# Optimization experiments

Hardware: AMD Instinct MI355X
Metric: run time of the kernel (lower is better)

The kernel has to match this reference:

```python
import jax, jax.numpy as jnp
import numpy as np

N_HEADS, N_LEVELS, N_POINTS, D_MODEL = 8, 4, 4, 256
HEAD_DIM = D_MODEL // N_HEADS
SHAPES = [(96, 96), (48, 48), (24, 24), (12, 12)]


def setup_inputs() -> dict:
    key = jax.random.key(0)
    ks = jax.random.split(key, 9)
    shapes_np = np.asarray(SHAPES, dtype=np.int32)
    lengths = shapes_np[:, 0] * shapes_np[:, 1]
    Len = int(lengths.sum())  # 12240
    B = 1
    level_start = np.concatenate([[0], np.cumsum(lengths)[:-1]]).astype(np.int32)
    return {
        "query": jax.random.normal(ks[0], (B, Len, D_MODEL), jnp.float32),
        "reference_points": jax.random.uniform(ks[1], (B, Len, 2), jnp.float32),
        "input_flatten": jax.random.normal(ks[2], (B, Len, D_MODEL), jnp.float32),
        "spatial_shapes": jnp.asarray(shapes_np),
        "level_start_index": jnp.asarray(level_start),
        "W_off": jax.random.normal(ks[3], (D_MODEL, N_HEADS * N_LEVELS * N_POINTS * 2), jnp.float32) * 0.01,
        "b_off": jax.random.normal(ks[4], (N_HEADS * N_LEVELS * N_POINTS * 2,), jnp.float32) * 0.01,
        "W_attn": jax.random.normal(ks[5], (D_MODEL, N_HEADS * N_LEVELS * N_POINTS), jnp.float32) * 0.02,
        "b_attn": jnp.zeros((N_HEADS * N_LEVELS * N_POINTS,), jnp.float32),
        "W_out": jax.random.normal(ks[6], (D_MODEL, D_MODEL), jnp.float32) * 0.02,
        "b_out": jnp.zeros((D_MODEL,), jnp.float32),
    }


def _bilinear_gather(feat, x, y, H, W):
    """feat: [B,nH,H*W,D]; x,y: [B,nH,S] pixel coords. Zero padding, align_corners=False."""
    x0 = jnp.floor(x)
    y0 = jnp.floor(y)
    wx1 = x - x0
    wy1 = y - y0
    wx0 = 1.0 - wx1
    wy0 = 1.0 - wy1
    x0i = x0.astype(jnp.int32)
    y0i = y0.astype(jnp.int32)

    def corner(ix, iy):
        valid = (ix >= 0) & (ix < W) & (iy >= 0) & (iy < H)
        idx = jnp.clip(iy, 0, H - 1) * W + jnp.clip(ix, 0, W - 1)
        g = jnp.take_along_axis(feat, idx[..., None], axis=2)  # [B,nH,S,D]
        return g * valid[..., None].astype(feat.dtype)

    return (corner(x0i, y0i) * (wx0 * wy0)[..., None]
            + corner(x0i + 1, y0i) * (wx1 * wy0)[..., None]
            + corner(x0i, y0i + 1) * (wx0 * wy1)[..., None]
            + corner(x0i + 1, y0i + 1) * (wx1 * wy1)[..., None])


def _ms_deform_core(value, shapes_np, loc, attn):
    """value: [B,Len_in,nH,D]; loc: [B,LQ,nH,nL,nP,2]; attn: [B,LQ,nH,nL,nP]."""
    B, LQ = loc.shape[0], loc.shape[1]
    lengths = [int(h) * int(w) for h, w in shapes_np]
    starts = np.concatenate([[0], np.cumsum(lengths)])
    out = jnp.zeros((B, N_HEADS, LQ, HEAD_DIM), value.dtype)
    for lvl, (H, W) in enumerate(shapes_np):
        H, W = int(H), int(W)
        feat = value[:, starts[lvl]:starts[lvl + 1]].transpose(0, 2, 1, 3)  # [B,nH,HW,D]
        l = loc[:, :, :, lvl]  # [B,LQ,nH,nP,2]
        x = (l[..., 0] * W - 0.5).transpose(0, 2, 1, 3).reshape(B, N_HEADS, LQ * N_POINTS)
        y = (l[..., 1] * H - 0.5).transpose(0, 2, 1, 3).reshape(B, N_HEADS, LQ * N_POINTS)
        samp = _bilinear_gather(feat, x, y, H, W).reshape(B, N_HEADS, LQ, N_POINTS, HEAD_DIM)
        w = attn[:, :, :, lvl].transpose(0, 2, 1, 3)  # [B,nH,LQ,nP]
        out = out + (samp * w[..., None]).sum(axis=3)
    return out.transpose(0, 2, 1, 3).reshape(B, LQ, N_HEADS * HEAD_DIM)


def reference(query, reference_points, input_flatten, spatial_shapes, level_start_index,
              W_off, b_off, W_attn, b_attn, W_out, b_out):
    B, LQ, C = query.shape
    shapes_np = np.asarray(spatial_shapes)  # static per-level (H,W)
    off = (query @ W_off + b_off).reshape(B, LQ, N_HEADS, N_LEVELS, N_POINTS, 2)
    attn = jax.nn.softmax((query @ W_attn + b_attn).reshape(B, LQ, N_HEADS, N_LEVELS * N_POINTS), axis=-1)
    attn = attn.reshape(B, LQ, N_HEADS, N_LEVELS, N_POINTS)
    # offset_normalizer = (W, H) per level
    norm = jnp.asarray(np.stack([shapes_np[:, 1], shapes_np[:, 0]], -1), dtype=query.dtype)
    loc = reference_points[:, :, None, None, None, :] + off / norm[None, None, None, :, None, :]
    value = input_flatten.reshape(B, -1, N_HEADS, HEAD_DIM)
    out = _ms_deform_core(value, shapes_np, loc, attn)
    return out @ W_out + b_out
```

## Files before the change

kernel.cpp:

```cpp
#include <hip/hip_runtime.h>
#include <hip/hip_bf16.h>
#include <math.h>

constexpr int D_MODEL  = 256;
constexpr int N_HEADS  = 8;

typedef __attribute__((ext_vector_type(8))) short bf16x8;
typedef __attribute__((ext_vector_type(4))) float f32x4;

__device__ __forceinline__ void gld_lds16(const void* gsrc, void* ldst) {
    __builtin_amdgcn_global_load_lds(
        (const __attribute__((address_space(1))) unsigned int*)gsrc,
        (__attribute__((address_space(3))) unsigned int*)ldst, 16, 0, 0);
}

__global__ __launch_bounds__(256) void convert_kernel(
    const float* __restrict__ q,
    const float* __restrict__ Woff,
    const float* __restrict__ Wattn,
    const float* __restrict__ Wout,
    __hip_bfloat16* __restrict__ qbf,
    __hip_bfloat16* __restrict__ wt,
    int M)
{
    int t = blockIdx.x * 256 + threadIdx.x;
    int nq4 = M * 64;
    if (t < nq4) {
        float4 v = reinterpret_cast<const float4*>(q)[t];
        union { __hip_bfloat16 h[4]; ushort4 u; } cv;
        cv.h[0] = __float2bfloat16(v.x);
        cv.h[1] = __float2bfloat16(v.y);
        cv.h[2] = __float2bfloat16(v.z);
        cv.h[3] = __float2bfloat16(v.w);
        reinterpret_cast<ushort4*>(qbf)[t] = cv.u;
    } else {
        int t2 = t - nq4;
        if (t2 < 640 * 256) {
            int c = t2 >> 8, k = t2 & 255;
            float val = (c < 256) ? Woff[k * 256 + c]
                      : (c < 384) ? Wattn[k * 128 + (c - 256)]
                                  : Wout[k * 256 + (c - 384)];
            wt[c * 256 + k] = __float2bfloat16(val);
        }
    }
}

template <int EPI>
__global__ __launch_bounds__(256) void gemm_mfma(
    const __hip_bfloat16* __restrict__ Abf,
    const __hip_bfloat16* __restrict__ Wt,
    int wrow0,
    const float* __restrict__ ba,
    const float* __restrict__ bb,
    const float* __restrict__ refpts,
    float* __restrict__ out0,
    float* __restrict__ out1,
    int M)
{
    __shared__ __align__(16) char smem[128 * 68 * 4];
    char*  A_lds = smem;
    char*  B_lds = smem + 16384;
    float* C_lds = (float*)smem;

    const int tid = threadIdx.x;
    const int w = tid >> 6, l = tid & 63;
    const int m0 = blockIdx.y * 128;
    const int n0 = blockIdx.x * 64;

    const char* Asrc = (const char*)Abf;
    const char* Wsrc = (const char*)(Wt + (size_t)(wrow0 + n0) * 256);

    f32x4 acc[2][4] = {};

    const int lr8 = l >> 3, l7 = l & 7;

    for (int k0 = 0; k0 < 512; k0 += 128) {
#pragma unroll
        for (int i = 0; i < 4; ++i) {
            int chunk = (w << 2) + i;
            int row = (chunk << 3) + lr8;
            int m = m0 + row; m = m < M ? m : (M - 1);
            gld_lds16(Asrc + (size_t)m * 512 + k0 + ((l7 ^ (row & 7)) << 4),
                      A_lds + (chunk << 10));
        }
#pragma unroll
        for (int i = 0; i < 2; ++i) {
            int chunk = (w << 1) + i;
            int row = (chunk << 3) + lr8;
            gld_lds16(Wsrc + (size_t)row * 512 + k0 + ((l7 ^ (row & 7)) << 4),
                      B_lds + (chunk << 10));
        }
        __syncthreads();

#pragma unroll
        for (int kk = 0; kk < 2; ++kk) {
            bf16x8 av[2], bv[4];
#pragma unroll
            for (int mf = 0; mf < 2; ++mf) {
                int arow = (w << 5) + (mf << 4) + (l & 15);
                int acb = ((kk << 6) + ((l >> 4) << 4)) ^ ((arow & 7) << 4);
                av[mf] = *(const bf16x8*)(A_lds + arow * 128 + acb);
            }
#pragma unroll
            for (int nf = 0; nf < 4; ++nf) {
                int brow = (nf << 4) + (l & 15);
                int bcb = ((kk << 6) + ((l >> 4) << 4)) ^ ((brow & 7) << 4);
                bv[nf] = *(const bf16x8*)(B_lds + brow * 128 + bcb);
            }
#pragma unroll
            for (int mf = 0; mf < 2; ++mf)
#pragma unroll
                for (int nf = 0; nf < 4; ++nf)
                    acc[mf][nf] = __builtin_amdgcn_mfma_f32_16x16x32_bf16(
                        av[mf], bv[nf], acc[mf][nf], 0, 0, 0);
        }
        __syncthreads();
    }

#pragma unroll
    for (int mf = 0; mf < 2; ++mf)
#pragma unroll
        for (int nf = 0; nf < 4; ++nf) {
            int col = (nf << 4) + (l & 15);
            int rbase = (w << 5) + (mf << 4) + ((l >> 4) << 2);
#pragma unroll
            for (int j = 0; j < 4; ++j)
                C_lds[(rbase + j) * 68 + col] = acc[mf][nf][j];
        }
    __syncthreads();

    if (EPI == 0 || n0 < 256) {
#pragma unroll
        for (int r2 = 0; r2 < 2; ++r2) {
            int row = (r2 << 6) + (tid >> 2);
            int q = m0 + row;
            if (q >= M) continue;
            float rx = 0.f, ry = 0.f;
            if (EPI == 1) { rx = refpts[q * 2]; ry = refpts[q * 2 + 1]; }
#pragma unroll
            for (int g = 0; g < 4; ++g) {
                int col = ((tid & 3) << 4) + (g << 2);
                float4 v  = *(float4*)&C_lds[row * 68 + col];
                float4 b4 = *(const float4*)&ba[n0 + col];
                if (EPI == 0) {
                    v.x += b4.x; v.y += b4.y; v.z += b4.z; v.w += b4.w;
                } else {
                    int c = n0 + col;
                    float rn = 1.0f / (float)(96 >> ((c >> 3) & 3));
                    v.x = rx + (v.x + b4.x) * rn;
                    v.y = ry + (v.y + b4.y) * rn;
                    v.z = rx + (v.z + b4.z) * rn;
                    v.w = ry + (v.w + b4.w) * rn;
                }
                *(float4*)&out0[(size_t)q * 256 + n0 + col] = v;
            }
        }
    } else {
        for (int u = tid; u < 512; u += 256) {
            int row = u >> 2, hh = u & 3;
            int q = m0 + row;
            if (q >= M) continue;
            int cg = (n0 - 256) + (hh << 4);
            float s[16];
            float mx = -1e30f;
#pragma unroll
            for (int i = 0; i < 16; ++i) {
                s[i] = C_lds[row * 68 + (hh << 4) + i] + bb[cg + i];
                mx = fmaxf(mx, s[i]);
            }
            float sum = 0.f;
#pragma unroll
            for (int i = 0; i < 16; ++i) { s[i] = __expf(s[i] - mx); sum += s[i]; }
            float inv = 1.0f / sum;
#pragma unroll
            for (int g = 0; g < 4; ++g) {
                float4 v = make_float4(s[g*4]*inv, s[g*4+1]*inv, s[g*4+2]*inv, s[g*4+3]*inv);
                *(float4*)&out1[(size_t)q * 128 + cg + (g << 2)] = v;
            }
        }
    }
}

__global__ __launch_bounds__(256, 4) void sample_kernel(
    const float* __restrict__ loc,
    const float* __restrict__ attn,
    const float* __restrict__ value,
    __hip_bfloat16* __restrict__ core,
    int M)
{
    const int unit = blockIdx.x * 32 + (threadIdx.x >> 3);
    const int d4   = threadIdx.x & 7;
    const int q    = unit >> 3;
    const int h    = unit & 7;
    if (q >= M) return;

    const float4* locq4 = reinterpret_cast<const float4*>(loc  + (size_t)q * 256 + h * 32);
    const float4* attq4 = reinterpret_cast<const float4*>(attn + (size_t)q * 128 + h * 16);
    const float*  vbase = value + h * 32 + d4 * 4;

    float4 acc = make_float4(0.f, 0.f, 0.f, 0.f);

#pragma unroll 1
    for (int lvl = 0; lvl < 4; ++lvl) {
        const int Wl = 96 >> lvl;
        const int start = 12288 - (12288 >> (2 * lvl));
        const float fW = (float)Wl;
        const int rowstride = Wl * 256;
        const float* feat = vbase + (size_t)start * 256;

        float4 lp0 = locq4[lvl * 2 + 0];
        float4 lp1 = locq4[lvl * 2 + 1];
        float4 aw  = attq4[lvl];

        const float lxs[4] = {lp0.x, lp0.z, lp1.x, lp1.z};
        const float lys[4] = {lp0.y, lp0.w, lp1.y, lp1.w};
        const float aws[4] = {aw.x, aw.y, aw.z, aw.w};

#pragma unroll
        for (int p = 0; p < 4; ++p) {
            float x = lxs[p] * fW - 0.5f;
            float y = lys[p] * fW - 0.5f;
            float wgt = aws[p];

            float x0f = floorf(x);
            float y0f = floorf(y);
            float wx1 = x - x0f, wy1 = y - y0f;
            float wx0 = 1.f - wx1, wy0 = 1.f - wy1;
            int ix = (int)x0f;
            int iy = (int)y0f;

            float wxv0 = ((unsigned)ix       < (unsigned)Wl) ? wx0 : 0.f;
            float wxv1 = ((unsigned)(ix + 1) < (unsigned)Wl) ? wx1 : 0.f;
            float wyv0 = (((unsigned)iy       < (unsigned)Wl) ? wy0 : 0.f) * wgt;
            float wyv1 = (((unsigned)(iy + 1) < (unsigned)Wl) ? wy1 : 0.f) * wgt;

            int ix0 = min(max(ix,     0), Wl - 1);
            int ix1 = min(max(ix + 1, 0), Wl - 1);
            int iy0 = min(max(iy,     0), Wl - 1);
            int iy1 = min(max(iy + 1, 0), Wl - 1);

            const float* row0 = feat + (size_t)iy0 * rowstride;
            const float* row1 = feat + (size_t)iy1 * rowstride;
            float4 v00 = *reinterpret_cast<const float4*>(&row0[(size_t)ix0 * 256]);
            float4 v10 = *reinterpret_cast<const float4*>(&row0[(size_t)ix1 * 256]);
            float4 v01 = *reinterpret_cast<const float4*>(&row1[(size_t)ix0 * 256]);
            float4 v11 = *reinterpret_cast<const float4*>(&row1[(size_t)ix1 * 256]);

            float w00 = wxv0 * wyv0, w10 = wxv1 * wyv0;
            float w01 = wxv0 * wyv1, w11 = wxv1 * wyv1;

            acc.x = fmaf(v00.x, w00, acc.x); acc.x = fmaf(v10.x, w10, acc.x);
            acc.x = fmaf(v01.x, w01, acc.x); acc.x = fmaf(v11.x, w11, acc.x);
            acc.y = fmaf(v00.y, w00, acc.y); acc.y = fmaf(v10.y, w10, acc.y);
            acc.y = fmaf(v01.y, w01, acc.y); acc.y = fmaf(v11.y, w11, acc.y);
            acc.z = fmaf(v00.z, w00, acc.z); acc.z = fmaf(v10.z, w10, acc.z);
            acc.z = fmaf(v01.z, w01, acc.z); acc.z = fmaf(v11.z, w11, acc.z);
            acc.w = fmaf(v00.w, w00, acc.w); acc.w = fmaf(v10.w, w10, acc.w);
            acc.w = fmaf(v01.w, w01, acc.w); acc.w = fmaf(v11.w, w11, acc.w);
        }
    }

    union { __hip_bfloat16 h4[4]; ushort4 u4; } st;
    st.h4[0] = __float2bfloat16(acc.x);
    st.h4[1] = __float2bfloat16(acc.y);
    st.h4[2] = __float2bfloat16(acc.z);
    st.h4[3] = __float2bfloat16(acc.w);
    *reinterpret_cast<ushort4*>(core + ((size_t)q * 256 + h * 32 + d4 * 4)) = st.u4;
}

extern "C" void kernel_launch(void* const* d_in, const int* in_sizes, int n_in,
                              void* d_out, int out_size, void* d_ws, size_t ws_size,
                              hipStream_t stream)
{
    const float* query  = (const float*)d_in[0];
    const float* refp   = (const float*)d_in[1];
    const float* value  = (const float*)d_in[2];
    const float* W_off  = (const float*)d_in[5];
    const float* b_off  = (const float*)d_in[6];
    const float* W_attn = (const float*)d_in[7];
    const float* b_attn = (const float*)d_in[8];
    const float* W_out  = (const float*)d_in[9];
    const float* b_out  = (const float*)d_in[10];
    float* out = (float*)d_out;

    const int M = in_sizes[0] / D_MODEL;

    float* loc  = (float*)d_ws;
    float* attn = loc + (size_t)M * 256;
    __hip_bfloat16* qbf = (__hip_bfloat16*)(attn + (size_t)M * 128);
    __hip_bfloat16* wt  = qbf + (size_t)M * 256;
    __hip_bfloat16* core = qbf;

    dim3 blk(256);
    const int mblocks = (M + 127) / 128;

    int convthreads = M * 64 + 640 * 256;
    hipLaunchKernelGGL(convert_kernel, dim3((convthreads + 255) / 256), blk, 0, stream,
                       query, W_off, W_attn, W_out, qbf, wt, M);

    hipLaunchKernelGGL((gemm_mfma<1>), dim3(6, mblocks), blk, 0, stream,
                       qbf, wt, 0, b_off, b_attn, refp, loc, attn, M);

    const int units = M * N_HEADS;
    hipLaunchKernelGGL(sample_kernel, dim3((units + 31) / 32), blk, 0, stream,
                       loc, attn, value, core, M);

    hipLaunchKernelGGL((gemm_mfma<0>), dim3(4, mblocks), blk, 0, stream,
                       core, wt, 384, b_out, nullptr, nullptr, out, nullptr, M);
}
```

Before: 73.57 us.

## Transpose value into per-head planes and schedule sampling blocks by head

The convert kernel now also copies the value tensor into a head-major layout, [head][pixel][32], so each head's features are contiguous. The sampling kernel reads from these planes and each block now handles one head for 32 consecutive queries, so a block's gathers stay in one compact plane that fits better in cache. The occupancy hint is raised from 4 to 8 blocks per CU. The cost is an extra full copy of the value tensor (about 12.5 MB read and written) on every call.

```diff
diff --git a/kernel.cpp b/kernel.cpp
--- a/kernel.cpp
+++ b/kernel.cpp
@@ -19,9 +19,11 @@
     const float* __restrict__ Woff,
     const float* __restrict__ Wattn,
     const float* __restrict__ Wout,
+    const float* __restrict__ value,
     __hip_bfloat16* __restrict__ qbf,
     __hip_bfloat16* __restrict__ wt,
-    int M)
+    float* __restrict__ vt,
+    int M, int Lv)
 {
     int t = blockIdx.x * 256 + threadIdx.x;
     int nq4 = M * 64;
@@ -33,15 +35,24 @@
         cv.h[2] = __float2bfloat16(v.z);
         cv.h[3] = __float2bfloat16(v.w);
         reinterpret_cast<ushort4*>(qbf)[t] = cv.u;
-    } else {
-        int t2 = t - nq4;
-        if (t2 < 640 * 256) {
-            int c = t2 >> 8, k = t2 & 255;
-            float val = (c < 256) ? Woff[k * 256 + c]
-                      : (c < 384) ? Wattn[k * 128 + (c - 256)]
-                                  : Wout[k * 256 + (c - 384)];
-            wt[c * 256 + k] = __float2bfloat16(val);
-        }
+        return;
+    }
+    int t2 = t - nq4;
+    if (t2 < 640 * 256) {
+        int c = t2 >> 8, k = t2 & 255;
+        float val = (c < 256) ? Woff[k * 256 + c]
+                  : (c < 384) ? Wattn[k * 128 + (c - 256)]
+                              : Wout[k * 256 + (c - 384)];
+        wt[c * 256 + k] = __float2bfloat16(val);
+        return;
+    }
+    int t3 = t2 - 640 * 256;
+    if (t3 < Lv * 64) {
+        int pix = t3 >> 6;
+        int c4  = (t3 & 63) * 4;
+        int h   = c4 >> 5, d = c4 & 31;
+        float4 v = reinterpret_cast<const float4*>(value)[t3];
+        *reinterpret_cast<float4*>(vt + (size_t)h * Lv * 32 + (size_t)pix * 32 + d) = v;
     }
 }
 
@@ -181,22 +192,23 @@
     }
 }
 
-__global__ __launch_bounds__(256, 4) void sample_kernel(
+__global__ __launch_bounds__(256, 8) void sample_kernel(
     const float* __restrict__ loc,
     const float* __restrict__ attn,
-    const float* __restrict__ value,
+    const float* __restrict__ vt,
     __hip_bfloat16* __restrict__ core,
-    int M)
+    int M, int Lv)
 {
-    const int unit = blockIdx.x * 32 + (threadIdx.x >> 3);
+    const int h    = blockIdx.x & 7;
+    const int q0   = (blockIdx.x >> 3) << 5;
+    const int unit = threadIdx.x >> 3;
     const int d4   = threadIdx.x & 7;
-    const int q    = unit >> 3;
-    const int h    = unit & 7;
+    const int q    = q0 + unit;
     if (q >= M) return;
 
     const float4* locq4 = reinterpret_cast<const float4*>(loc  + (size_t)q * 256 + h * 32);
     const float4* attq4 = reinterpret_cast<const float4*>(attn + (size_t)q * 128 + h * 16);
-    const float*  vbase = value + h * 32 + d4 * 4;
+    const float*  plane = vt + (size_t)h * Lv * 32 + d4 * 4;
 
     float4 acc = make_float4(0.f, 0.f, 0.f, 0.f);
 
@@ -205,8 +217,8 @@
         const int Wl = 96 >> lvl;
         const int start = 12288 - (12288 >> (2 * lvl));
         const float fW = (float)Wl;
-        const int rowstride = Wl * 256;
-        const float* feat = vbase + (size_t)start * 256;
+        const int rowstride = Wl * 32;
+        const float* feat = plane + (size_t)start * 32;
 
         float4 lp0 = locq4[lvl * 2 + 0];
         float4 lp1 = locq4[lvl * 2 + 1];
@@ -241,10 +253,10 @@
 
             const float* row0 = feat + (size_t)iy0 * rowstride;
             const float* row1 = feat + (size_t)iy1 * rowstride;
-            float4 v00 = *reinterpret_cast<const float4*>(&row0[(size_t)ix0 * 256]);
-            float4 v10 = *reinterpret_cast<const float4*>(&row0[(size_t)ix1 * 256]);
-            float4 v01 = *reinterpret_cast<const float4*>(&row1[(size_t)ix0 * 256]);
-            float4 v11 = *reinterpret_cast<const float4*>(&row1[(size_t)ix1 * 256]);
+            float4 v00 = *reinterpret_cast<const float4*>(&row0[ix0 * 32]);
+            float4 v10 = *reinterpret_cast<const float4*>(&row0[ix1 * 32]);
+            float4 v01 = *reinterpret_cast<const float4*>(&row1[ix0 * 32]);
+            float4 v11 = *reinterpret_cast<const float4*>(&row1[ix1 * 32]);
 
             float w00 = wxv0 * wyv0, w10 = wxv1 * wyv0;
             float w01 = wxv0 * wyv1, w11 = wxv1 * wyv1;
@@ -283,27 +295,29 @@
     const float* b_out  = (const float*)d_in[10];
     float* out = (float*)d_out;
 
-    const int M = in_sizes[0] / D_MODEL;
+    const int M  = in_sizes[0] / D_MODEL;
+    const int Lv = in_sizes[2] / D_MODEL;
 
     float* loc  = (float*)d_ws;
     float* attn = loc + (size_t)M * 256;
     __hip_bfloat16* qbf = (__hip_bfloat16*)(attn + (size_t)M * 128);
     __hip_bfloat16* wt  = qbf + (size_t)M * 256;
+    float* vt = (float*)(wt + 640 * 256);
     __hip_bfloat16* core = qbf;
 
     dim3 blk(256);
     const int mblocks = (M + 127) / 128;
 
-    int convthreads = M * 64 + 640 * 256;
+    int convthreads = M * 64 + 640 * 256 + Lv * 64;
     hipLaunchKernelGGL(convert_kernel, dim3((convthreads + 255) / 256), blk, 0, stream,
-                       query, W_off, W_attn, W_out, qbf, wt, M);
+                       query, W_off, W_attn, W_out, value, qbf, wt, vt, M, Lv);
 
     hipLaunchKernelGGL((gemm_mfma<1>), dim3(6, mblocks), blk, 0, stream,
                        qbf, wt, 0, b_off, b_attn, refp, loc, attn, M);
 
-    const int units = M * N_HEADS;
-    hipLaunchKernelGGL(sample_kernel, dim3((units + 31) / 32), blk, 0, stream,
-                       loc, attn, value, core, M);
+    const int qchunks = (M + 31) / 32;
+    hipLaunchKernelGGL(sample_kernel, dim3(qchunks * 8), blk, 0, stream,
+                       loc, attn, vt, core, M, Lv);
 
     hipLaunchKernelGGL((gemm_mfma<0>), dim3(4, mblocks), blk, 0, stream,
                        core, wt, 384, b_out, nullptr, nullptr, out, nullptr, M);
```

Result: no change. 74.76 us (+1.6%).
